# Kernel optimization log

Hardware: AMD Instinct MI355X
Metric: run time of the kernel (lower is better)

## Reference

```python
import jax, jax.numpy as jnp
import numpy as np
import math

B, S, E, H = 2, 2048, 1024, 16
D = E // H
# neuromodulator levels (deterministic branch choices)
NA, ACH, DA = 0.5, 0.5, -0.5

def setup_inputs() -> dict:
    key = jax.random.key(0)
    ks = jax.random.split(key, 12)
    xav = lambda k, i, o: jax.random.uniform(k, (i, o), jnp.float32, -1.0, 1.0) * math.sqrt(6.0 / (i + o))
    return {
        'query': jax.random.normal(ks[0], (B, S, E), jnp.float32),
        'key':   jax.random.normal(ks[1], (B, S, E), jnp.float32),
        'value': jax.random.normal(ks[2], (B, S, E), jnp.float32),
        'Wq': xav(ks[3], E, E), 'bq': jnp.zeros((E,), jnp.float32),
        'Wk': xav(ks[4], E, E), 'bk': jnp.zeros((E,), jnp.float32),
        'Wv': xav(ks[5], E, E), 'bv': jnp.zeros((E,), jnp.float32),
        'Wo': xav(ks[6], E, E), 'bo': jnp.zeros((E,), jnp.float32),
        'time_scales': jnp.ones((H,), jnp.float32),
    }

def reference(query, key, value, Wq, bq, Wk, bk, Wv, bv, Wo, bo, time_scales):
    # projections -> [B, H, S, D]
    q = (query @ Wq + bq).reshape(B, S, H, D).transpose(0, 2, 1, 3)
    k = (key   @ Wk + bk).reshape(B, S, H, D).transpose(0, 2, 1, 3)
    v = (value @ Wv + bv).reshape(B, S, H, D).transpose(0, 2, 1, 3)
    # per-head time-scale on keys
    k = k * time_scales[None, :, None, None]
    scores = jnp.einsum('bhtd,bhsd->bhts', q, k) / math.sqrt(D)
    # noradrenaline: temperature scaling
    temperature = 1.0 / (1.0 + NA * 0.5)
    scores = scores / temperature
    # acetylcholine: boost diagonal
    diag = jnp.eye(S, dtype=scores.dtype)[None, None]
    scores = scores * (1.0 + ACH * 0.3 * diag)
    kk = max(1, int(S * 0.2))
    topv = jax.lax.top_k(scores, kk)[0]          # [B,H,S,kk]
    min_topk = topv[..., -1:]                     # kth largest
    mask = (scores >= min_topk).astype(scores.dtype)
    scores = scores * (1.0 + (-DA) * 0.3 * mask)
    attn = jax.nn.softmax(scores, axis=-1)
    out = jnp.einsum('bhts,bhsd->bhtd', attn, v)
    out = out.transpose(0, 2, 1, 3).reshape(B, S, E)
    out = out @ Wo + bo
    return out
```

## Files before the change

kernel.cpp:

```cpp
#include <hip/hip_runtime.h>
#include <cstdint>
#include <cstddef>

#define BB 2
#define SS 2048
#define EE 1024
#define HH 16
#define DH 64
#define KKSEL 409
#define QT 16
#define PST 136

typedef __attribute__((ext_vector_type(8))) short bf16x8;
typedef __attribute__((ext_vector_type(4))) float f32x4;
typedef unsigned short ushort_t;

__device__ __forceinline__ unsigned short f2bf(float f){
    unsigned u = __float_as_uint(f);
    u += 0x7fffu + ((u >> 16) & 1u);
    return (unsigned short)(u >> 16);
}
__device__ __forceinline__ float bf2f(unsigned short h){
    return __uint_as_float(((unsigned)h) << 16);
}
__device__ __forceinline__ unsigned sortkey(float f){
    unsigned u = __float_as_uint(f);
    return (u & 0x80000000u) ? ~u : (u | 0x80000000u);
}
__device__ __forceinline__ float inv_sortkey(unsigned k){
    unsigned u = (k & 0x80000000u) ? (k & 0x7fffffffu) : ~k;
    return __uint_as_float(u);
}
__device__ __forceinline__ void split8(const float* f, bf16x8& h, bf16x8& l){
    #pragma unroll
    for (int j = 0; j < 8; ++j){
        ushort_t hh = f2bf(f[j]);
        h[j] = (short)hh;
        l[j] = (short)f2bf(f[j] - bf2f(hh));
    }
}
__device__ __forceinline__ void gload_lds16(const ushort_t* g, ushort_t* l){
    __builtin_amdgcn_global_load_lds(
        (const __attribute__((address_space(1))) void*)g,
        (__attribute__((address_space(3))) void*)l, 16, 0, 0);
}

struct CvtArgs {
    const float* W[4];
    ushort_t* H[4];
    ushort_t* L[4];
};

__global__ __launch_bounds__(256) void convert_wt4(CvtArgs a)
{
    __shared__ float T[64][65];
    const int z = blockIdx.z;
    const float* __restrict__ W = a.W[z];
    ushort_t* __restrict__ Ht = a.H[z];
    ushort_t* __restrict__ Lt = a.L[z];

    const int tid = threadIdx.x;
    const int ty = tid >> 4, tx = tid & 15;
    const int n0 = blockIdx.x * 64, k0 = blockIdx.y * 64;
    #pragma unroll
    for (int i = 0; i < 4; ++i){
        const int kl = ty + i * 16;
        float4 w = *(const float4*)&W[(size_t)(k0 + kl) * EE + n0 + tx * 4];
        T[kl][tx*4 + 0] = w.x; T[kl][tx*4 + 1] = w.y;
        T[kl][tx*4 + 2] = w.z; T[kl][tx*4 + 3] = w.w;
    }
    __syncthreads();
    #pragma unroll
    for (int i = 0; i < 4; ++i){
        const int nl = ty + i * 16;
        ushort4 h, l;
        ushort_t* hp = &h.x; ushort_t* lp = &l.x;
        #pragma unroll
        for (int j = 0; j < 4; ++j){
            const float v = T[tx*4 + j][nl];
            ushort_t hh = f2bf(v);
            hp[j] = hh;
            lp[j] = f2bf(v - bf2f(hh));
        }
        const size_t o = (size_t)(n0 + nl) * EE + k0 + tx * 4;
        *(ushort4*)&Ht[o] = h;
        *(ushort4*)&Lt[o] = l;
    }
}

struct CvtX {
    const float* X[3];
    ushort_t* H[3];
    ushort_t* L[3];
};

__global__ __launch_bounds__(256) void convert_x3(CvtX a)
{
    const int z = blockIdx.z;
    const float* __restrict__ X = a.X[z];
    ushort_t* __restrict__ Hd = a.H[z];
    ushort_t* __restrict__ Ld = a.L[z];
    const size_t i = ((size_t)blockIdx.x * 256 + threadIdx.x) * 8;
    float fx[8];
    *(float4*)&fx[0] = *(const float4*)&X[i];
    *(float4*)&fx[4] = *(const float4*)&X[i + 4];
    bf16x8 h, l;
    split8(fx, h, l);
    *(bf16x8*)&Hd[i] = h;
    *(bf16x8*)&Ld[i] = l;
}

template<int MODE>
__device__ __forceinline__ void gemm_body(
        const ushort_t* __restrict__ Xh, const ushort_t* __restrict__ Xl,
        const ushort_t* __restrict__ Wth, const ushort_t* __restrict__ Wtl,
        const float* __restrict__ bias, const float* __restrict__ ts,
        float* __restrict__ OutF, ushort_t* __restrict__ OutH,
        ushort_t* __restrict__ OutL, ushort_t* buf, int bx, int by)
{
    const int tid  = threadIdx.x;
    const int lane = tid & 63, wave = tid >> 6;
    const int c16  = lane & 15, qd = lane >> 4;
    const int m0 = by * 128, n0 = bx * 64;
    const int wm = (wave >> 1) * 64, wn = (wave & 1) * 32;

    f32x4 acc[8];
    #pragma unroll
    for (int i = 0; i < 8; ++i) acc[i] = (f32x4){0.f,0.f,0.f,0.f};

    const int seg0 = wave * 2, seg1 = seg0 + 1;
    const int rl = lane >> 2, kl = (lane & 3) * 8;
    const size_t xofs0 = (size_t)(m0 + seg0*16 + rl) * EE + kl;
    const size_t xofs1 = (size_t)(m0 + seg1*16 + rl) * EE + kl;
    const size_t wofs = (size_t)(n0 + wave*16 + rl) * EE + kl;

    for (int k0 = 0; k0 < EE; k0 += 32){
        gload_lds16(Xh  + xofs0 + k0, buf +         seg0*512);
        gload_lds16(Xh  + xofs1 + k0, buf +         seg1*512);
        gload_lds16(Xl  + xofs0 + k0, buf + 4096  + seg0*512);
        gload_lds16(Xl  + xofs1 + k0, buf + 4096  + seg1*512);
        gload_lds16(Wth + wofs  + k0, buf + 8192  + wave*512);
        gload_lds16(Wtl + wofs  + k0, buf + 10240 + wave*512);
        __syncthreads();

        const ushort_t* A0 = buf;
        const ushort_t* A1 = buf + 4096;
        const ushort_t* B0 = buf + 8192;
        const ushort_t* B1 = buf + 10240;
        bf16x8 afh[4], afl[4], bfh[2], bfl[2];
        #pragma unroll
        for (int i = 0; i < 4; ++i){
            afh[i] = *(const bf16x8*)&A0[(wm + i*16 + c16)*32 + qd*8];
            afl[i] = *(const bf16x8*)&A1[(wm + i*16 + c16)*32 + qd*8];
        }
        #pragma unroll
        for (int j = 0; j < 2; ++j){
            bfh[j] = *(const bf16x8*)&B0[(wn + j*16 + c16)*32 + qd*8];
            bfl[j] = *(const bf16x8*)&B1[(wn + j*16 + c16)*32 + qd*8];
        }
        if (MODE == 2){
            #pragma unroll
            for (int ma = 0; ma < 4; ++ma){
                #pragma unroll
                for (int nb = 0; nb < 2; ++nb){
                    const int id = ma*2 + nb;
                    acc[id] = __builtin_amdgcn_mfma_f32_16x16x32_bf16(afh[ma], bfh[nb], acc[id], 0,0,0);
                    acc[id] = __builtin_amdgcn_mfma_f32_16x16x32_bf16(afh[ma], bfl[nb], acc[id], 0,0,0);
                    acc[id] = __builtin_amdgcn_mfma_f32_16x16x32_bf16(afl[ma], bfh[nb], acc[id], 0,0,0);
                }
            }
        } else {
            #pragma unroll
            for (int na = 0; na < 2; ++na){
                #pragma unroll
                for (int mb = 0; mb < 4; ++mb){
                    const int id = na*4 + mb;
                    acc[id] = __builtin_amdgcn_mfma_f32_16x16x32_bf16(bfh[na], afh[mb], acc[id], 0,0,0);
                    acc[id] = __builtin_amdgcn_mfma_f32_16x16x32_bf16(bfh[na], afl[mb], acc[id], 0,0,0);
                    acc[id] = __builtin_amdgcn_mfma_f32_16x16x32_bf16(bfl[na], afh[mb], acc[id], 0,0,0);
                }
            }
        }
        if (k0 + 32 < EE) __syncthreads();
    }

    if (MODE == 3){
        #pragma unroll
        for (int na = 0; na < 2; ++na){
            const int ng = n0 + wn + na*16 + qd*4;
            float4 b4 = *(const float4*)&bias[ng];
            const float bb[4] = {b4.x, b4.y, b4.z, b4.w};
            #pragma unroll
            for (int mb = 0; mb < 4; ++mb){
                const int mg = m0 + wm + mb*16 + c16;
                const f32x4 av = acc[na*4 + mb];
                float4 o;
                o.x = av[0] + bb[0]; o.y = av[1] + bb[1];
                o.z = av[2] + bb[2]; o.w = av[3] + bb[3];
                *(float4*)&OutF[(size_t)mg * EE + ng] = o;
            }
        }
    } else if (MODE == 0){
        #pragma unroll
        for (int na = 0; na < 2; ++na){
            const int ng = n0 + wn + na*16 + qd*4;
            const int h = ng >> 6, d0 = ng & 63;
            float4 b4 = *(const float4*)&bias[ng];
            const float bb[4] = {b4.x, b4.y, b4.z, b4.w};
            #pragma unroll
            for (int mb = 0; mb < 4; ++mb){
                const int mg = m0 + wm + mb*16 + c16;
                const int bi = mg >> 11, s = mg & (SS - 1);
                const f32x4 av = acc[na*4 + mb];
                ushort4 hv, lv;
                ushort_t* hp = &hv.x; ushort_t* lp = &lv.x;
                #pragma unroll
                for (int r = 0; r < 4; ++r){
                    const float v = av[r] + bb[r];
                    ushort_t hh = f2bf(v);
                    hp[r] = hh;
                    lp[r] = f2bf(v - bf2f(hh));
                }
                const size_t o = (((size_t)(bi * HH + h)) * SS + s) * DH + d0;
                *(ushort4*)&OutH[o] = hv;
                *(ushort4*)&OutL[o] = lv;
            }
        }
    } else if (MODE == 1){
        #pragma unroll
        for (int na = 0; na < 2; ++na){
            const int ng = n0 + wn + na*16 + qd*4;
            const int h = ng >> 6, d0 = ng & 63;
            const float tsc = ts[h];
            float4 b4 = *(const float4*)&bias[ng];
            const float bb[4] = {b4.x, b4.y, b4.z, b4.w};
            #pragma unroll
            for (int mb = 0; mb < 4; ++mb){
                const int mg = m0 + wm + mb*16 + c16;
                const int bi = mg >> 11, s = mg & (SS - 1);
                const f32x4 av = acc[na*4 + mb];
                ushort4 hv;
                ushort_t* hp = &hv.x;
                #pragma unroll
                for (int r = 0; r < 4; ++r)
                    hp[r] = f2bf((av[r] + bb[r]) * tsc);
                *(ushort4*)&OutH[(((size_t)(bi * HH + h)) * SS + s) * DH + d0] = hv;
            }
        }
    } else {
        #pragma unroll
        for (int ma = 0; ma < 4; ++ma){
            const int mg = m0 + wm + ma*16 + qd*4;
            const int bi = mg >> 11, s0 = mg & (SS - 1);
            #pragma unroll
            for (int nb = 0; nb < 2; ++nb){
                const int ng = n0 + wn + nb*16 + c16;
                const int h = ng >> 6, d = ng & 63;
                const float bv = bias[ng];
                const f32x4 av = acc[ma*2 + nb];
                ushort4 hv;
                ushort_t* hp = &hv.x;
                #pragma unroll
                for (int r = 0; r < 4; ++r) hp[r] = f2bf(av[r] + bv);
                *(ushort4*)&OutH[(((size_t)(bi * HH + h)) * DH + d) * SS + s0] = hv;
            }
        }
    }
}

__device__ __forceinline__ void panel_swizzle(int& bx, int& by){
    const int lin = blockIdx.x + 16 * blockIdx.y;
    const int xcd = lin & 7, idx = lin >> 3;
    bx = idx & 15;
    by = (xcd << 2) | (idx >> 4);
}

__global__ __launch_bounds__(256) void gemm_qkv(
        const ushort_t* __restrict__ Xqh, const ushort_t* __restrict__ Xql,
        const ushort_t* __restrict__ Xkh, const ushort_t* __restrict__ Xkl,
        const ushort_t* __restrict__ Xvh, const ushort_t* __restrict__ Xvl,
        const ushort_t* __restrict__ Wqh, const ushort_t* __restrict__ Wql,
        const ushort_t* __restrict__ Wkh, const ushort_t* __restrict__ Wkl,
        const ushort_t* __restrict__ Wvh, const ushort_t* __restrict__ Wvl,
        const float* __restrict__ bq, const float* __restrict__ bk,
        const float* __restrict__ bv, const float* __restrict__ ts,
        ushort_t* __restrict__ Qh, ushort_t* __restrict__ Ql,
        ushort_t* __restrict__ Kh, ushort_t* __restrict__ Vth)
{
    __shared__ ushort_t buf[12288];
    int bx, by;
    panel_swizzle(bx, by);
    const int z = blockIdx.z;
    if (z == 0)
        gemm_body<0>(Xqh, Xql, Wqh, Wql, bq, nullptr, nullptr, Qh, Ql, buf, bx, by);
    else if (z == 1)
        gemm_body<1>(Xkh, Xkl, Wkh, Wkl, bk, ts, nullptr, Kh, nullptr, buf, bx, by);
    else
        gemm_body<2>(Xvh, Xvl, Wvh, Wvl, bv, nullptr, nullptr, Vth, nullptr, buf, bx, by);
}

__global__ __launch_bounds__(256) void gemm_out(
        const ushort_t* __restrict__ AOh, const ushort_t* __restrict__ AOl,
        const ushort_t* __restrict__ Wth, const ushort_t* __restrict__ Wtl,
        const float* __restrict__ bias, float* __restrict__ OutF)
{
    __shared__ ushort_t buf[12288];
    int bx, by;
    panel_swizzle(bx, by);
    gemm_body<3>(AOh, AOl, Wth, Wtl, bias, nullptr, OutF, nullptr, nullptr, buf, bx, by);
}

__global__ __launch_bounds__(512, 4) void attn_kernel(
        const ushort_t* __restrict__ Qh, const ushort_t* __restrict__ Ql,
        const ushort_t* __restrict__ Khi, const ushort_t* __restrict__ Vth,
        ushort_t* __restrict__ AOh, ushort_t* __restrict__ AOl)
{
    __shared__ __align__(16) char uni[65536];
    __shared__ float wsums[8][16];
    __shared__ unsigned thr16[16];

    const int tid  = threadIdx.x;
    const int lane = tid & 63;
    const int wave = tid >> 6;
    const int qd   = lane >> 4;
    const int c16  = lane & 15;
    const unsigned Bx = blockIdx.x;
    const int xcd  = Bx & 7;
    const int qq   = Bx >> 3;
    const int tile = qq & 127;
    const int bh   = (qq >> 7) * 8 + xcd;
    const int t0   = tile * QT;
    const int wbase = wave * 256;

    bf16x8 qh[2], ql[2];
    {
        const size_t qbase = ((size_t)bh * SS + t0 + c16) * DH;
        #pragma unroll
        for (int kc = 0; kc < 2; ++kc){
            qh[kc] = *(const bf16x8*)&Qh[qbase + kc*32 + qd*8];
            ql[kc] = *(const bf16x8*)&Ql[qbase + kc*32 + qd*8];
        }
    }

    f32x4 acc[16];
    const ushort_t* Kh = Khi + (size_t)bh * SS * DH;
    #pragma unroll
    for (int t = 0; t < 16; ++t){
        f32x4 a = {0.f, 0.f, 0.f, 0.f};
        const int srow = wbase + t*16 + c16;
        const ushort_t* kp = Kh + (size_t)srow * DH + qd*8;
        #pragma unroll
        for (int kc = 0; kc < 2; ++kc){
            bf16x8 kh = *(const bf16x8*)(kp + kc*32);
            a = __builtin_amdgcn_mfma_f32_16x16x32_bf16(qh[kc], kh, a, 0, 0, 0);
            a = __builtin_amdgcn_mfma_f32_16x16x32_bf16(ql[kc], kh, a, 0, 0, 0);
        }
        acc[t] = a;
    }

    #pragma unroll
    for (int t = 0; t < 16; ++t){
        const int colg = wbase + t*16 + c16;
        #pragma unroll
        for (int r = 0; r < 4; ++r){
            float v = acc[t][r] * 0.15625f;
            if (colg == t0 + qd*4 + r) v *= 1.15f;
            acc[t][r] = __uint_as_float(sortkey(v));
        }
    }

    float* ex = (float*)uni;
    #pragma unroll
    for (int half = 0; half < 2; ++half){
        if ((qd >> 1) == half){
            const int rl = (qd & 1) * 4;
            #pragma unroll
            for (int t = 0; t < 16; ++t)
                #pragma unroll
                for (int r = 0; r < 4; ++r)
                    ex[(rl + r) * SS + wbase + t*16 + c16] = acc[t][r];
        }
        __syncthreads();
        unsigned cand[32];
        #pragma unroll
        for (int j = 0; j < 32; ++j)
            cand[j] = __float_as_uint(ex[wave * SS + lane + 64*j]);
        unsigned kmn = cand[0], kmx = cand[0];
        #pragma unroll
        for (int j = 1; j < 32; ++j){
            kmn = (cand[j] < kmn) ? cand[j] : kmn;
            kmx = (cand[j] > kmx) ? cand[j] : kmx;
        }
        #pragma unroll
        for (int off = 1; off < 64; off <<= 1){
            const unsigned on = (unsigned)__shfl_xor((int)kmn, off, 64);
            const unsigned ox = (unsigned)__shfl_xor((int)kmx, off, 64);
            kmn = (on < kmn) ? on : kmn;
            kmx = (ox > kmx) ? ox : kmx;
        }
        unsigned lo = kmn, hi = kmx + 1u;
        #pragma unroll 1
        for (int it = 0; it < 32 && (hi - lo) > 1u; ++it){
            const unsigned mid = lo + ((hi - lo) >> 1);
            int c = 0;
            #pragma unroll
            for (int j = 0; j < 32; ++j){
                int pc;
                asm("v_cmp_le_u32 vcc, %1, %2\n\t"
                    "s_bcnt1_i32_b64 %0, vcc"
                    : "=s"(pc) : "s"(mid), "v"(cand[j]) : "vcc");
                c += pc;
            }
            if (c == KKSEL){ lo = mid; break; }
            if (c > KKSEL) lo = mid; else hi = mid;
        }
        if (lane == 0) thr16[half*8 + wave] = lo;
        __syncthreads();
    }

    unsigned thr[4];
    #pragma unroll
    for (int r = 0; r < 4; ++r) thr[r] = thr16[qd*4 + r];
    float psum[4] = {0.f, 0.f, 0.f, 0.f};
    #pragma unroll
    for (int t = 0; t < 16; ++t){
        #pragma unroll
        for (int r = 0; r < 4; ++r){
            const unsigned key = __float_as_uint(acc[t][r]);
            float s = inv_sortkey(key);
            s *= (key >= thr[r]) ? 1.15f : 1.0f;
            const float e = __expf(s);
            acc[t][r] = e;
            psum[r] += e;
        }
    }
    #pragma unroll
    for (int off = 1; off <= 8; off <<= 1){
        #pragma unroll
        for (int r = 0; r < 4; ++r) psum[r] += __shfl_xor(psum[r], off, 64);
    }
    if (c16 == 0){
        #pragma unroll
        for (int r = 0; r < 4; ++r) wsums[wave][qd*4 + r] = psum[r];
    }
    __syncthreads();
    float pinv[4];
    #pragma unroll
    for (int r = 0; r < 4; ++r){
        const int row = qd*4 + r;
        float s = 0.f;
        #pragma unroll
        for (int w = 0; w < 8; ++w) s += wsums[w][row];
        pinv[r] = 1.f / s;
    }

    const ushort_t* Vh = Vth + (size_t)bh * DH * SS;
    ushort_t* pw = (ushort_t*)uni + wave * (QT * PST);
    f32x4 oacc[4];
    #pragma unroll
    for (int dt = 0; dt < 4; ++dt) oacc[dt] = (f32x4){0.f, 0.f, 0.f, 0.f};

    #pragma unroll
    for (int half = 0; half < 2; ++half){
        #pragma unroll
        for (int tt = 0; tt < 8; ++tt){
            const int t = half*8 + tt;
            #pragma unroll
            for (int r = 0; r < 4; ++r)
                pw[(qd*4 + r) * PST + tt*16 + c16] = f2bf(acc[t][r] * pinv[r]);
        }
        #pragma unroll
        for (int kc = 0; kc < 4; ++kc){
            bf16x8 pf = *(const bf16x8*)&pw[c16 * PST + kc*32 + qd*8];
            const int sbase = wbase + half*128 + kc*32 + qd*8;
            #pragma unroll
            for (int dt = 0; dt < 4; ++dt){
                const int d = dt*16 + c16;
                bf16x8 vh = *(const bf16x8*)(Vh + (size_t)d * SS + sbase);
                oacc[dt] = __builtin_amdgcn_mfma_f32_16x16x32_bf16(pf, vh, oacc[dt], 0, 0, 0);
            }
        }
    }

    __syncthreads();
    float* red = (float*)uni;
    #pragma unroll
    for (int dt = 0; dt < 4; ++dt)
        #pragma unroll
        for (int r = 0; r < 4; ++r)
            red[(wave*16 + qd*4 + r) * 65 + dt*16 + c16] = oacc[dt][r];
    __syncthreads();

    const int b = bh >> 4, h = bh & 15;
    {
        const int r  = tid >> 5;
        const int c2 = (tid & 31) * 2;
        float s0 = 0.f, s1 = 0.f;
        #pragma unroll
        for (int w = 0; w < 8; ++w){
            s0 += red[(w*16 + r) * 65 + c2];
            s1 += red[(w*16 + r) * 65 + c2 + 1];
        }
        const size_t o = ((size_t)b * SS + t0 + r) * EE + h*DH + c2;
        ushort2 hv, lv;
        hv.x = f2bf(s0); lv.x = f2bf(s0 - bf2f(hv.x));
        hv.y = f2bf(s1); lv.y = f2bf(s1 - bf2f(hv.y));
        *(ushort2*)&AOh[o] = hv;
        *(ushort2*)&AOl[o] = lv;
    }
}

extern "C" void kernel_launch(void* const* d_in, const int* in_sizes, int n_in,
                              void* d_out, int out_size, void* d_ws, size_t ws_size,
                              hipStream_t stream)
{
    const float* query = (const float*)d_in[0];
    const float* key   = (const float*)d_in[1];
    const float* value = (const float*)d_in[2];
    const float* Wq    = (const float*)d_in[3];
    const float* bq    = (const float*)d_in[4];
    const float* Wk    = (const float*)d_in[5];
    const float* bk    = (const float*)d_in[6];
    const float* Wv    = (const float*)d_in[7];
    const float* bv    = (const float*)d_in[8];
    const float* Wo    = (const float*)d_in[9];
    const float* bo    = (const float*)d_in[10];
    const float* ts    = (const float*)d_in[11];
    float* out = (float*)d_out;
    char* w = (char*)d_ws;

    const size_t MB = 1u << 20;
    ushort_t* Qh  = (ushort_t*)(w + 0 * MB);
    ushort_t* Ql  = (ushort_t*)(w + 8 * MB);
    ushort_t* Kh  = (ushort_t*)(w + 16 * MB);
    ushort_t* Vth = (ushort_t*)(w + 24 * MB);
    ushort_t* Wqh = (ushort_t*)(w + 32 * MB);
    ushort_t* Wql = (ushort_t*)(w + 34 * MB);
    ushort_t* Wkh = (ushort_t*)(w + 36 * MB);
    ushort_t* Wkl = (ushort_t*)(w + 38 * MB);
    ushort_t* Wvh = (ushort_t*)(w + 40 * MB);
    ushort_t* Wvl = (ushort_t*)(w + 42 * MB);
    ushort_t* Woh = (ushort_t*)(w + 44 * MB);
    ushort_t* Wol = (ushort_t*)(w + 46 * MB);
    ushort_t* Xqh = (ushort_t*)(w + 48 * MB);
    ushort_t* Xql = (ushort_t*)(w + 56 * MB);
    ushort_t* Xkh = (ushort_t*)(w + 64 * MB);
    ushort_t* Xkl = (ushort_t*)(w + 72 * MB);
    ushort_t* Xvh = (ushort_t*)(w + 80 * MB);
    ushort_t* Xvl = (ushort_t*)(w + 88 * MB);
    ushort_t* AOh = (ushort_t*)(w + 48 * MB);
    ushort_t* AOl = (ushort_t*)(w + 56 * MB);

    CvtArgs ca;
    ca.W[0] = Wq;  ca.W[1] = Wk;  ca.W[2] = Wv;  ca.W[3] = Wo;
    ca.H[0] = Wqh; ca.H[1] = Wkh; ca.H[2] = Wvh; ca.H[3] = Woh;
    ca.L[0] = Wql; ca.L[1] = Wkl; ca.L[2] = Wvl; ca.L[3] = Wol;

    CvtX cx;
    cx.X[0] = query; cx.X[1] = key; cx.X[2] = value;
    cx.H[0] = Xqh;   cx.H[1] = Xkh; cx.H[2] = Xvh;
    cx.L[0] = Xql;   cx.L[1] = Xkl; cx.L[2] = Xvl;

    hipLaunchKernelGGL(convert_wt4, dim3(16, 16, 4), dim3(256), 0, stream, ca);
    hipLaunchKernelGGL(convert_x3, dim3(2048, 1, 3), dim3(256), 0, stream, cx);
    hipLaunchKernelGGL(gemm_qkv, dim3(16, 32, 3), dim3(256), 0, stream,
                       Xqh, Xql, Xkh, Xkl, Xvh, Xvl,
                       Wqh, Wql, Wkh, Wkl, Wvh, Wvl,
                       bq, bk, bv, ts, Qh, Ql, Kh, Vth);
    hipLaunchKernelGGL(attn_kernel, dim3(BB * HH * (SS / QT)), dim3(512), 0, stream,
                       Qh, Ql, Kh, Vth, AOh, AOl);
    hipLaunchKernelGGL(gemm_out, dim3(16, 32), dim3(256), 0, stream,
                       AOh, AOl, Woh, Wol, bo, out);
}
```

Measured before the change: 641.8 us.

## Double-buffer LDS tiles in projection GEMMs to overlap loads with MFMA

The shared GEMM body now holds two LDS stages. The global-to-LDS load for the next K tile is issued before the MFMA work on the current tile, so each iteration needs one barrier instead of two. The goal is to hide global memory latency behind compute in the QKV and output projection GEMMs. The cost is doubled LDS per block, 48 KB instead of 24 KB, which may limit how many blocks fit on a CU at once.

```diff
diff --git a/kernel.cpp b/kernel.cpp
--- a/kernel.cpp
+++ b/kernel.cpp
@@ -134,19 +134,28 @@
     const size_t xofs1 = (size_t)(m0 + seg1*16 + rl) * EE + kl;
     const size_t wofs = (size_t)(n0 + wave*16 + rl) * EE + kl;
 
+    auto stage = [&](ushort_t* S, int kt){
+        gload_lds16(Xh  + xofs0 + kt, S +         seg0*512);
+        gload_lds16(Xh  + xofs1 + kt, S +         seg1*512);
+        gload_lds16(Xl  + xofs0 + kt, S + 4096  + seg0*512);
+        gload_lds16(Xl  + xofs1 + kt, S + 4096  + seg1*512);
+        gload_lds16(Wth + wofs  + kt, S + 8192  + wave*512);
+        gload_lds16(Wtl + wofs  + kt, S + 10240 + wave*512);
+    };
+
+    stage(buf, 0);
+    __syncthreads();
+
+    int cur = 0;
     for (int k0 = 0; k0 < EE; k0 += 32){
-        gload_lds16(Xh  + xofs0 + k0, buf +         seg0*512);
-        gload_lds16(Xh  + xofs1 + k0, buf +         seg1*512);
-        gload_lds16(Xl  + xofs0 + k0, buf + 4096  + seg0*512);
-        gload_lds16(Xl  + xofs1 + k0, buf + 4096  + seg1*512);
-        gload_lds16(Wth + wofs  + k0, buf + 8192  + wave*512);
-        gload_lds16(Wtl + wofs  + k0, buf + 10240 + wave*512);
-        __syncthreads();
-
-        const ushort_t* A0 = buf;
-        const ushort_t* A1 = buf + 4096;
-        const ushort_t* B0 = buf + 8192;
-        const ushort_t* B1 = buf + 10240;
+        const bool more = (k0 + 32) < EE;
+        if (more) stage(buf + (cur ^ 1) * 12288, k0 + 32);
+
+        const ushort_t* S  = buf + cur * 12288;
+        const ushort_t* A0 = S;
+        const ushort_t* A1 = S + 4096;
+        const ushort_t* B0 = S + 8192;
+        const ushort_t* B1 = S + 10240;
         bf16x8 afh[4], afl[4], bfh[2], bfl[2];
         #pragma unroll
         for (int i = 0; i < 4; ++i){
@@ -181,7 +190,10 @@
                 }
             }
         }
-        if (k0 + 32 < EE) __syncthreads();
+        if (more){
+            __syncthreads();
+            cur ^= 1;
+        }
     }
 
     if (MODE == 3){
@@ -287,7 +299,7 @@
         ushort_t* __restrict__ Qh, ushort_t* __restrict__ Ql,
         ushort_t* __restrict__ Kh, ushort_t* __restrict__ Vth)
 {
-    __shared__ ushort_t buf[12288];
+    __shared__ ushort_t buf[2 * 12288];
     int bx, by;
     panel_swizzle(bx, by);
     const int z = blockIdx.z;
@@ -304,7 +316,7 @@
         const ushort_t* __restrict__ Wth, const ushort_t* __restrict__ Wtl,
         const float* __restrict__ bias, float* __restrict__ OutF)
 {
-    __shared__ ushort_t buf[12288];
+    __shared__ ushort_t buf[2 * 12288];
     int bx, by;
     panel_swizzle(bx, by);
     gemm_body<3>(AOh, AOl, Wth, Wtl, bias, nullptr, OutF, nullptr, nullptr, buf, bx, by);
```

Measured after the change: 657.4 us. +2.4%, slower.
